# Kernel optimization log

Hardware: AMD Instinct MI355X
Metric: run time of the kernel (lower is better)

Reference implementation:

```python
import jax, jax.numpy as jnp
import numpy as np

DT = 0.1  # fixed RK4 step size from the constructor

def setup_inputs() -> dict:
    key = jax.random.key(0)
    k1, k2, k3 = jax.random.split(key, 3)
    B, U, H = 65536, 128, 512
    x0 = jax.random.normal(k1, (B, U), dtype=jnp.float32)
    # small init so 20 unrolled RK4 steps stay numerically tame
    W1 = jax.random.normal(k2, (U, H), dtype=jnp.float32) * (0.5 / np.sqrt(U))
    b1 = jnp.zeros((H,), dtype=jnp.float32)
    W2 = jax.random.normal(k3, (H, U), dtype=jnp.float32) * (0.5 / np.sqrt(H))
    b2 = jnp.zeros((U,), dtype=jnp.float32)
    return {"x0": x0, "W1": W1, "b1": b1, "W2": W2, "b2": b2}

def _mlp(x, W1, b1, W2, b2):
    # vector field: Dense(512, relu) -> Dense(128); time-independent
    return jnp.maximum(x @ W1 + b1, 0.0) @ W2 + b2

def _rk4_integrate(x, n_steps, W1, b1, W2, b2):
    def step(x, _):
        k1 = _mlp(x, W1, b1, W2, b2)
        k2 = _mlp(x + 0.5 * DT * k1, W1, b1, W2, b2)
        k3 = _mlp(x + 0.5 * DT * k2, W1, b1, W2, b2)
        k4 = _mlp(x + DT * k3, W1, b1, W2, b2)
        return x + (DT / 6.0) * (k1 + 2.0 * k2 + 2.0 * k3 + k4), None
    x, _ = jax.lax.scan(step, x, None, length=n_steps)
    return x

def reference(x0, W1, b1, W2, b2):
    # phase 1: integrate t in [0, t1/2 = 1.0] -> 10 RK4 steps at dt=0.1
    x = _rk4_integrate(x0, 10, W1, b1, W2, b2)
    # phase 2: n=5 macro-steps of length (1.0 - 0.0)/5 = 0.2 -> 2 RK4 steps each
    def macro(x, _):
        x = _rk4_integrate(x, 2, W1, b1, W2, b2)
        return x, None
    x, _ = jax.lax.scan(macro, x, None, length=5)
    return x
```

## Files before the change

### kernel.cpp

```cpp
#include <hip/hip_runtime.h>
#include <stdint.h>


typedef _Float16 half8 __attribute__((ext_vector_type(8)));
typedef float f32x4 __attribute__((ext_vector_type(4)));
typedef __attribute__((address_space(3))) char lchar;
typedef __attribute__((address_space(1))) char gchar;

#define XSTR 136
#define HSTR 40

static __device__ __forceinline__ void gload_lds16(const void* g, void* l) {
  __builtin_amdgcn_global_load_lds((const gchar*)g, (lchar*)l, 16, 0, 0);
}

static __device__ __forceinline__ unsigned short f2h(float x) {
  union { _Float16 h; unsigned short u; } cv;
  cv.h = (_Float16)x;
  return cv.u;
}
static __device__ __forceinline__ float h2f(unsigned short u) {
  union { unsigned short u; _Float16 h; } cv;
  cv.u = u;
  return (float)cv.h;
}
static __device__ __forceinline__ uint64_t pack4(float a, float b, float c, float d) {
  union { _Float16 h[4]; uint64_t q; } cv;
  cv.h[0] = (_Float16)a; cv.h[1] = (_Float16)b;
  cv.h[2] = (_Float16)c; cv.h[3] = (_Float16)d;
  return cv.q;
}

__global__ void pack_w(const float* __restrict__ W1, const float* __restrict__ W2,
                       unsigned short* __restrict__ wp) {
  int id = blockIdx.x * 256 + threadIdx.x;
  int lane = id & 63, fid = (id >> 6) & 255;
  int g = lane >> 4, lm = lane & 15;
  int c = fid >> 4, f = fid & 15;
  if (f < 8) {
    int T = f >> 2, ks = f & 3;
    int hid = c * 32 + T * 16 + lm;
#pragma unroll
    for (int j = 0; j < 8; ++j) {
      int kin = ks * 32 + g * 8 + j;
      wp[fid * 512 + lane * 8 + j] = f2h(W1[kin * 512 + hid]);
    }
  } else {
    int O = f - 8;
    int of = O * 16 + lm;
#pragma unroll
    for (int j = 0; j < 8; ++j) {
      int kh = c * 32 + g * 8 + j;
      wp[fid * 512 + lane * 8 + j] = f2h(W2[kh * 128 + of]);
    }
  }
}

__global__ __launch_bounds__(512, 2) void node_rk4(
    const float* __restrict__ x0, const float* __restrict__ b1,
    const float* __restrict__ b2, const unsigned short* __restrict__ wp,
    float* __restrict__ out) {
  __shared__ char Wbuf[4][16384];
  __shared__ __align__(16) unsigned short xs[8][32][XSTR];
  __shared__ __align__(16) unsigned short hst[8][32][HSTR];
  __shared__ float b1s[512];
  __shared__ float b2s[128];

  const int tid = threadIdx.x;
  const int w = tid >> 6, lane = tid & 63;
  const int g = lane >> 4, lm = lane & 15;

  b1s[tid] = b1[tid];
  if (tid < 128) b2s[tid] = b2[tid];

  const int rbase = blockIdx.x * 256 + w * 32;
  f32x4 xa[2][8];
  ushort4 xbh[2][8];
#pragma unroll
  for (int nt = 0; nt < 2; ++nt)
#pragma unroll
    for (int O = 0; O < 8; ++O) {
      f32x4 v = *(const f32x4*)&x0[(rbase + nt * 16 + lm) * 128 + O * 16 + 4 * g];
      xa[nt][O] = v;
      uint64_t q = pack4(v[0], v[1], v[2], v[3]);
      ushort4 hq;
      *(uint64_t*)&hq = q;
      xbh[nt][O] = hq;
      *(uint64_t*)&xs[w][nt * 16 + lm][O * 16 + 4 * g] = q;
    }

#pragma unroll
  for (int pc = 0; pc < 2; ++pc) {
    const char* src = (const char*)wp + pc * 16384;
#pragma unroll
    for (int q = 0; q < 2; ++q) {
      int seg = w * 2 + q;
      gload_lds16(src + seg * 1024 + lane * 16, Wbuf[pc] + seg * 1024);
    }
  }
  asm volatile("s_waitcnt vmcnt(2) lgkmcnt(0)" ::: "memory");
  __builtin_amdgcn_s_barrier();

#pragma unroll 1
  for (int it = 0; it < 80; ++it) {
    const int s = it & 3;
    const float wgt = (s == 0 || s == 3) ? (0.1f / 6.0f) : (0.1f / 3.0f);
    const float alph = (s < 2) ? 0.05f : 0.1f;

    half8 X1[2][4];
#pragma unroll
    for (int nt = 0; nt < 2; ++nt)
#pragma unroll
      for (int ks = 0; ks < 4; ++ks)
        X1[nt][ks] = *(const half8*)&xs[w][nt * 16 + lm][ks * 32 + g * 8];

    f32x4 yacc[2][8];
#pragma unroll
    for (int nt = 0; nt < 2; ++nt)
#pragma unroll
      for (int O = 0; O < 8; ++O) yacc[nt][O] = f32x4{0.f, 0.f, 0.f, 0.f};

#pragma unroll
    for (int c = 0; c < 16; ++c) {
      half8 Hp0, Hp1;
      if (c > 0) {
        Hp0 = *(const half8*)&hst[w][lm][g * 8];
        Hp1 = *(const half8*)&hst[w][16 + lm][g * 8];
      }

      {
        const int cn = (c + 2) & 15;
        char* buf = Wbuf[(c + 2) & 3];
        const char* src = (const char*)wp + cn * 16384;
#pragma unroll
        for (int q = 0; q < 2; ++q) {
          int seg = w * 2 + q;
          gload_lds16(src + seg * 1024 + lane * 16, buf + seg * 1024);
        }
      }

      __builtin_amdgcn_s_setprio(1);
      if (c > 0) {
        const char* Wp = Wbuf[(c + 3) & 3];
#pragma unroll
        for (int O = 0; O < 8; ++O) {
          half8 wa = *(const half8*)(Wp + 8192 + O * 1024 + lane * 16);
          yacc[0][O] = __builtin_amdgcn_mfma_f32_16x16x32_f16(wa, Hp0, yacc[0][O], 0, 0, 0);
          yacc[1][O] = __builtin_amdgcn_mfma_f32_16x16x32_f16(wa, Hp1, yacc[1][O], 0, 0, 0);
        }
      }

      const char* Wb = Wbuf[c & 3];
#pragma unroll
      for (int T = 0; T < 2; ++T) {
        f32x4 h0 = {0.f, 0.f, 0.f, 0.f}, h1 = {0.f, 0.f, 0.f, 0.f};
#pragma unroll
        for (int ks = 0; ks < 4; ++ks) {
          half8 wa = *(const half8*)(Wb + (T * 4 + ks) * 1024 + lane * 16);
          h0 = __builtin_amdgcn_mfma_f32_16x16x32_f16(wa, X1[0][ks], h0, 0, 0, 0);
          h1 = __builtin_amdgcn_mfma_f32_16x16x32_f16(wa, X1[1][ks], h1, 0, 0, 0);
        }
        __builtin_amdgcn_s_setprio(0);
        f32x4 bb = *(const f32x4*)&b1s[c * 32 + T * 16 + 4 * g];
        uint64_t p0 = pack4(fmaxf(h0[0] + bb[0], 0.f), fmaxf(h0[1] + bb[1], 0.f),
                            fmaxf(h0[2] + bb[2], 0.f), fmaxf(h0[3] + bb[3], 0.f));
        uint64_t p1 = pack4(fmaxf(h1[0] + bb[0], 0.f), fmaxf(h1[1] + bb[1], 0.f),
                            fmaxf(h1[2] + bb[2], 0.f), fmaxf(h1[3] + bb[3], 0.f));
        *(uint64_t*)&hst[w][lm][T * 16 + 4 * g] = p0;
        *(uint64_t*)&hst[w][16 + lm][T * 16 + 4 * g] = p1;
        __builtin_amdgcn_s_setprio(1);
      }
      __builtin_amdgcn_s_setprio(0);

      asm volatile("s_waitcnt vmcnt(2)" ::: "memory");
      __builtin_amdgcn_s_barrier();
    }

    {
      half8 Hl0 = *(const half8*)&hst[w][lm][g * 8];
      half8 Hl1 = *(const half8*)&hst[w][16 + lm][g * 8];
      const char* Wp = Wbuf[3];
#pragma unroll
      for (int O = 0; O < 8; ++O) {
        half8 wa = *(const half8*)(Wp + 8192 + O * 1024 + lane * 16);
        yacc[0][O] = __builtin_amdgcn_mfma_f32_16x16x32_f16(wa, Hl0, yacc[0][O], 0, 0, 0);
        yacc[1][O] = __builtin_amdgcn_mfma_f32_16x16x32_f16(wa, Hl1, yacc[1][O], 0, 0, 0);
      }
    }

#pragma unroll
    for (int nt = 0; nt < 2; ++nt)
#pragma unroll
      for (int O = 0; O < 8; ++O) {
        f32x4 bb2 = *(const f32x4*)&b2s[O * 16 + 4 * g];
        f32x4 k = yacc[nt][O];
#pragma unroll
        for (int j = 0; j < 4; ++j) k[j] += bb2[j];
        xa[nt][O] += wgt * k;
        uint64_t q;
        if (s == 3) {
          f32x4 v = xa[nt][O];
          q = pack4(v[0], v[1], v[2], v[3]);
          ushort4 hq;
          *(uint64_t*)&hq = q;
          xbh[nt][O] = hq;
        } else {
          ushort4 xq = xbh[nt][O];
          q = pack4(h2f(xq.x) + alph * k[0], h2f(xq.y) + alph * k[1],
                    h2f(xq.z) + alph * k[2], h2f(xq.w) + alph * k[3]);
        }
        *(uint64_t*)&xs[w][nt * 16 + lm][O * 16 + 4 * g] = q;
      }
  }

#pragma unroll
  for (int nt = 0; nt < 2; ++nt)
#pragma unroll
    for (int O = 0; O < 8; ++O)
      *(f32x4*)&out[(rbase + nt * 16 + lm) * 128 + O * 16 + 4 * g] = xa[nt][O];
}

extern "C" void kernel_launch(void* const* d_in, const int* in_sizes, int n_in,
                              void* d_out, int out_size, void* d_ws, size_t ws_size,
                              hipStream_t stream) {
  const float* x0 = (const float*)d_in[0];
  const float* W1 = (const float*)d_in[1];
  const float* b1 = (const float*)d_in[2];
  const float* W2 = (const float*)d_in[3];
  const float* b2 = (const float*)d_in[4];
  float* out = (float*)d_out;

  unsigned short* wp = (unsigned short*)d_ws;

  pack_w<<<64, 256, 0, stream>>>(W1, W2, wp);
  node_rk4<<<256, 512, 0, stream>>>(x0, b1, b2, wp, out);
}
```

Before: 1.930 ms.

## Switch MFMA tiles from 16x16x32 to 32x32x16 with repacked weight layout

Replaces the 16x16x32 f16 MFMA tiling with 32x32x16 MFMAs for both MLP layers. The weight packing, the accumulator layout, the x and hidden LDS indexing, and the output mapping are all rewritten to match the 32-row fragment layout. Larger MFMA tiles halve the instruction count and cut LDS operand traffic per FLOP. In exchange, each wave needs more accumulator registers and the epilogue layout changes.

```diff
diff --git a/kernel.cpp b/kernel.cpp
--- a/kernel.cpp
+++ b/kernel.cpp
@@ -4,6 +4,7 @@
 
 typedef _Float16 half8 __attribute__((ext_vector_type(8)));
 typedef float f32x4 __attribute__((ext_vector_type(4)));
+typedef float f32x16 __attribute__((ext_vector_type(16)));
 typedef __attribute__((address_space(3))) char lchar;
 typedef __attribute__((address_space(1))) char gchar;
 
@@ -35,22 +36,21 @@
                        unsigned short* __restrict__ wp) {
   int id = blockIdx.x * 256 + threadIdx.x;
   int lane = id & 63, fid = (id >> 6) & 255;
-  int g = lane >> 4, lm = lane & 15;
+  int n32 = lane & 31, hi = lane >> 5;
   int c = fid >> 4, f = fid & 15;
   if (f < 8) {
-    int T = f >> 2, ks = f & 3;
-    int hid = c * 32 + T * 16 + lm;
+    int hid = c * 32 + n32;
 #pragma unroll
     for (int j = 0; j < 8; ++j) {
-      int kin = ks * 32 + g * 8 + j;
+      int kin = f * 16 + hi * 8 + j;
       wp[fid * 512 + lane * 8 + j] = f2h(W1[kin * 512 + hid]);
     }
   } else {
-    int O = f - 8;
-    int of = O * 16 + lm;
+    int u = f - 8, O = u >> 1, kf = u & 1;
+    int of = O * 32 + n32;
 #pragma unroll
     for (int j = 0; j < 8; ++j) {
-      int kh = c * 32 + g * 8 + j;
+      int kh = c * 32 + kf * 16 + hi * 8 + j;
       wp[fid * 512 + lane * 8 + j] = f2h(W2[kh * 128 + of]);
     }
   }
@@ -68,25 +68,25 @@
 
   const int tid = threadIdx.x;
   const int w = tid >> 6, lane = tid & 63;
-  const int g = lane >> 4, lm = lane & 15;
+  const int n32 = lane & 31, hi = lane >> 5;
 
   b1s[tid] = b1[tid];
   if (tid < 128) b2s[tid] = b2[tid];
 
   const int rbase = blockIdx.x * 256 + w * 32;
-  f32x4 xa[2][8];
-  ushort4 xbh[2][8];
-#pragma unroll
-  for (int nt = 0; nt < 2; ++nt)
-#pragma unroll
-    for (int O = 0; O < 8; ++O) {
-      f32x4 v = *(const f32x4*)&x0[(rbase + nt * 16 + lm) * 128 + O * 16 + 4 * g];
-      xa[nt][O] = v;
-      uint64_t q = pack4(v[0], v[1], v[2], v[3]);
+  f32x4 xa[4][4];
+  ushort4 xbh[4][4];
+#pragma unroll
+  for (int O = 0; O < 4; ++O)
+#pragma unroll
+    for (int q = 0; q < 4; ++q) {
+      f32x4 v = *(const f32x4*)&x0[(rbase + n32) * 128 + O * 32 + 8 * q + 4 * hi];
+      xa[O][q] = v;
+      uint64_t qq = pack4(v[0], v[1], v[2], v[3]);
       ushort4 hq;
-      *(uint64_t*)&hq = q;
-      xbh[nt][O] = hq;
-      *(uint64_t*)&xs[w][nt * 16 + lm][O * 16 + 4 * g] = q;
+      *(uint64_t*)&hq = qq;
+      xbh[O][q] = hq;
+      *(uint64_t*)&xs[w][n32][O * 32 + 8 * q + 4 * hi] = qq;
     }
 
 #pragma unroll
@@ -107,25 +107,23 @@
     const float wgt = (s == 0 || s == 3) ? (0.1f / 6.0f) : (0.1f / 3.0f);
     const float alph = (s < 2) ? 0.05f : 0.1f;
 
-    half8 X1[2][4];
-#pragma unroll
-    for (int nt = 0; nt < 2; ++nt)
-#pragma unroll
-      for (int ks = 0; ks < 4; ++ks)
-        X1[nt][ks] = *(const half8*)&xs[w][nt * 16 + lm][ks * 32 + g * 8];
-
-    f32x4 yacc[2][8];
-#pragma unroll
-    for (int nt = 0; nt < 2; ++nt)
-#pragma unroll
-      for (int O = 0; O < 8; ++O) yacc[nt][O] = f32x4{0.f, 0.f, 0.f, 0.f};
+    half8 X1[8];
+#pragma unroll
+    for (int ks = 0; ks < 8; ++ks)
+      X1[ks] = *(const half8*)&xs[w][n32][ks * 16 + hi * 8];
+
+    f32x16 yacc[4];
+#pragma unroll
+    for (int O = 0; O < 4; ++O)
+#pragma unroll
+      for (int e = 0; e < 16; ++e) yacc[O][e] = 0.f;
 
 #pragma unroll
     for (int c = 0; c < 16; ++c) {
       half8 Hp0, Hp1;
       if (c > 0) {
-        Hp0 = *(const half8*)&hst[w][lm][g * 8];
-        Hp1 = *(const half8*)&hst[w][16 + lm][g * 8];
+        Hp0 = *(const half8*)&hst[w][n32][hi * 8];
+        Hp1 = *(const half8*)&hst[w][n32][16 + hi * 8];
       }
 
       {
@@ -143,81 +141,82 @@
       if (c > 0) {
         const char* Wp = Wbuf[(c + 3) & 3];
 #pragma unroll
-        for (int O = 0; O < 8; ++O) {
-          half8 wa = *(const half8*)(Wp + 8192 + O * 1024 + lane * 16);
-          yacc[0][O] = __builtin_amdgcn_mfma_f32_16x16x32_f16(wa, Hp0, yacc[0][O], 0, 0, 0);
-          yacc[1][O] = __builtin_amdgcn_mfma_f32_16x16x32_f16(wa, Hp1, yacc[1][O], 0, 0, 0);
+        for (int O = 0; O < 4; ++O) {
+          half8 wa0 = *(const half8*)(Wp + 8192 + (O * 2 + 0) * 1024 + lane * 16);
+          half8 wa1 = *(const half8*)(Wp + 8192 + (O * 2 + 1) * 1024 + lane * 16);
+          yacc[O] = __builtin_amdgcn_mfma_f32_32x32x16_f16(wa0, Hp0, yacc[O], 0, 0, 0);
+          yacc[O] = __builtin_amdgcn_mfma_f32_32x32x16_f16(wa1, Hp1, yacc[O], 0, 0, 0);
         }
       }
 
       const char* Wb = Wbuf[c & 3];
-#pragma unroll
-      for (int T = 0; T < 2; ++T) {
-        f32x4 h0 = {0.f, 0.f, 0.f, 0.f}, h1 = {0.f, 0.f, 0.f, 0.f};
-#pragma unroll
-        for (int ks = 0; ks < 4; ++ks) {
-          half8 wa = *(const half8*)(Wb + (T * 4 + ks) * 1024 + lane * 16);
-          h0 = __builtin_amdgcn_mfma_f32_16x16x32_f16(wa, X1[0][ks], h0, 0, 0, 0);
-          h1 = __builtin_amdgcn_mfma_f32_16x16x32_f16(wa, X1[1][ks], h1, 0, 0, 0);
-        }
-        __builtin_amdgcn_s_setprio(0);
-        f32x4 bb = *(const f32x4*)&b1s[c * 32 + T * 16 + 4 * g];
-        uint64_t p0 = pack4(fmaxf(h0[0] + bb[0], 0.f), fmaxf(h0[1] + bb[1], 0.f),
-                            fmaxf(h0[2] + bb[2], 0.f), fmaxf(h0[3] + bb[3], 0.f));
-        uint64_t p1 = pack4(fmaxf(h1[0] + bb[0], 0.f), fmaxf(h1[1] + bb[1], 0.f),
-                            fmaxf(h1[2] + bb[2], 0.f), fmaxf(h1[3] + bb[3], 0.f));
-        *(uint64_t*)&hst[w][lm][T * 16 + 4 * g] = p0;
-        *(uint64_t*)&hst[w][16 + lm][T * 16 + 4 * g] = p1;
-        __builtin_amdgcn_s_setprio(1);
+      f32x16 hacc;
+#pragma unroll
+      for (int e = 0; e < 16; ++e) hacc[e] = 0.f;
+#pragma unroll
+      for (int ks = 0; ks < 8; ++ks) {
+        half8 wa = *(const half8*)(Wb + ks * 1024 + lane * 16);
+        hacc = __builtin_amdgcn_mfma_f32_32x32x16_f16(wa, X1[ks], hacc, 0, 0, 0);
       }
       __builtin_amdgcn_s_setprio(0);
+
+#pragma unroll
+      for (int q = 0; q < 4; ++q) {
+        f32x4 bb = *(const f32x4*)&b1s[c * 32 + 8 * q + 4 * hi];
+        uint64_t p = pack4(fmaxf(hacc[4 * q + 0] + bb[0], 0.f),
+                           fmaxf(hacc[4 * q + 1] + bb[1], 0.f),
+                           fmaxf(hacc[4 * q + 2] + bb[2], 0.f),
+                           fmaxf(hacc[4 * q + 3] + bb[3], 0.f));
+        *(uint64_t*)&hst[w][n32][8 * q + 4 * hi] = p;
+      }
 
       asm volatile("s_waitcnt vmcnt(2)" ::: "memory");
       __builtin_amdgcn_s_barrier();
     }
 
     {
-      half8 Hl0 = *(const half8*)&hst[w][lm][g * 8];
-      half8 Hl1 = *(const half8*)&hst[w][16 + lm][g * 8];
+      half8 Hl0 = *(const half8*)&hst[w][n32][hi * 8];
+      half8 Hl1 = *(const half8*)&hst[w][n32][16 + hi * 8];
       const char* Wp = Wbuf[3];
 #pragma unroll
-      for (int O = 0; O < 8; ++O) {
-        half8 wa = *(const half8*)(Wp + 8192 + O * 1024 + lane * 16);
-        yacc[0][O] = __builtin_amdgcn_mfma_f32_16x16x32_f16(wa, Hl0, yacc[0][O], 0, 0, 0);
-        yacc[1][O] = __builtin_amdgcn_mfma_f32_16x16x32_f16(wa, Hl1, yacc[1][O], 0, 0, 0);
-      }
-    }
-
-#pragma unroll
-    for (int nt = 0; nt < 2; ++nt)
-#pragma unroll
-      for (int O = 0; O < 8; ++O) {
-        f32x4 bb2 = *(const f32x4*)&b2s[O * 16 + 4 * g];
-        f32x4 k = yacc[nt][O];
-#pragma unroll
-        for (int j = 0; j < 4; ++j) k[j] += bb2[j];
-        xa[nt][O] += wgt * k;
-        uint64_t q;
+      for (int O = 0; O < 4; ++O) {
+        half8 wa0 = *(const half8*)(Wp + 8192 + (O * 2 + 0) * 1024 + lane * 16);
+        half8 wa1 = *(const half8*)(Wp + 8192 + (O * 2 + 1) * 1024 + lane * 16);
+        yacc[O] = __builtin_amdgcn_mfma_f32_32x32x16_f16(wa0, Hl0, yacc[O], 0, 0, 0);
+        yacc[O] = __builtin_amdgcn_mfma_f32_32x32x16_f16(wa1, Hl1, yacc[O], 0, 0, 0);
+      }
+    }
+
+#pragma unroll
+    for (int O = 0; O < 4; ++O)
+#pragma unroll
+      for (int q = 0; q < 4; ++q) {
+        f32x4 bb2 = *(const f32x4*)&b2s[O * 32 + 8 * q + 4 * hi];
+        f32x4 k;
+#pragma unroll
+        for (int j = 0; j < 4; ++j) k[j] = yacc[O][4 * q + j] + bb2[j];
+        xa[O][q] += wgt * k;
+        uint64_t qq;
         if (s == 3) {
-          f32x4 v = xa[nt][O];
-          q = pack4(v[0], v[1], v[2], v[3]);
+          f32x4 v = xa[O][q];
+          qq = pack4(v[0], v[1], v[2], v[3]);
           ushort4 hq;
-          *(uint64_t*)&hq = q;
-          xbh[nt][O] = hq;
+          *(uint64_t*)&hq = qq;
+          xbh[O][q] = hq;
         } else {
-          ushort4 xq = xbh[nt][O];
-          q = pack4(h2f(xq.x) + alph * k[0], h2f(xq.y) + alph * k[1],
-                    h2f(xq.z) + alph * k[2], h2f(xq.w) + alph * k[3]);
+          ushort4 xq = xbh[O][q];
+          qq = pack4(h2f(xq.x) + alph * k[0], h2f(xq.y) + alph * k[1],
+                     h2f(xq.z) + alph * k[2], h2f(xq.w) + alph * k[3]);
         }
-        *(uint64_t*)&xs[w][nt * 16 + lm][O * 16 + 4 * g] = q;
+        *(uint64_t*)&xs[w][n32][O * 32 + 8 * q + 4 * hi] = qq;
       }
   }
 
 #pragma unroll
-  for (int nt = 0; nt < 2; ++nt)
-#pragma unroll
-    for (int O = 0; O < 8; ++O)
-      *(f32x4*)&out[(rbase + nt * 16 + lm) * 128 + O * 16 + 4 * g] = xa[nt][O];
+  for (int O = 0; O < 4; ++O)
+#pragma unroll
+    for (int q = 0; q < 4; ++q)
+      *(f32x4*)&out[(rbase + n32) * 128 + O * 32 + 8 * q + 4 * hi] = xa[O][q];
 }
 
 extern "C" void kernel_launch(void* const* d_in, const int* in_sizes, int n_in,
```

Result: slower. 2.156 ms (+11.7%).

## Give each wave 64 rows with 4 waves per block and swizzle LDS tiles

Applied to the files above, without the earlier changes.

Blocks shrink from 8 waves to 4, and each wave now processes 64 batch rows instead of 32, so every weight fragment read from LDS feeds four MFMAs instead of two. The LDS tiles for x and h drop their padded strides in favor of an XOR swizzle to avoid bank conflicts, and the s_setprio hints are removed. The cost is much higher register pressure from the larger accumulator, x and hidden arrays. Fewer waves are also available to hide the per-chunk barrier and global-to-LDS weight loads, and register spills are possible.

```diff
diff --git a/kernel.cpp b/kernel.cpp
--- a/kernel.cpp
+++ b/kernel.cpp
@@ -6,9 +6,6 @@
 typedef float f32x4 __attribute__((ext_vector_type(4)));
 typedef __attribute__((address_space(3))) char lchar;
 typedef __attribute__((address_space(1))) char gchar;
-
-#define XSTR 136
-#define HSTR 40
 
 static __device__ __forceinline__ void gload_lds16(const void* g, void* l) {
   __builtin_amdgcn_global_load_lds((const gchar*)g, (lchar*)l, 16, 0, 0);
@@ -29,6 +26,13 @@
   cv.h[0] = (_Float16)a; cv.h[1] = (_Float16)b;
   cv.h[2] = (_Float16)c; cv.h[3] = (_Float16)d;
   return cv.q;
+}
+
+static __device__ __forceinline__ int xs_off(int r, int feat) {
+  return (r * 272 + feat * 2) ^ ((r & 8) << 1);
+}
+static __device__ __forceinline__ int hs_off(int r, int hid) {
+  return (r * 80 + hid * 2) ^ ((r & 8) << 1);
 }
 
 __global__ void pack_w(const float* __restrict__ W1, const float* __restrict__ W2,
@@ -56,28 +60,31 @@
   }
 }
 
-__global__ __launch_bounds__(512, 2) void node_rk4(
+__global__ __launch_bounds__(256, 1) void node_rk4(
     const float* __restrict__ x0, const float* __restrict__ b1,
     const float* __restrict__ b2, const unsigned short* __restrict__ wp,
     float* __restrict__ out) {
   __shared__ char Wbuf[4][16384];
-  __shared__ __align__(16) unsigned short xs[8][32][XSTR];
-  __shared__ __align__(16) unsigned short hst[8][32][HSTR];
+  __shared__ __align__(16) char xsm[4][64 * 272];
+  __shared__ __align__(16) char hsm[4][64 * 80];
   __shared__ float b1s[512];
   __shared__ float b2s[128];
 
   const int tid = threadIdx.x;
   const int w = tid >> 6, lane = tid & 63;
   const int g = lane >> 4, lm = lane & 15;
+  char* xsw = xsm[w];
+  char* hsw = hsm[w];
 
   b1s[tid] = b1[tid];
+  b1s[tid + 256] = b1[tid + 256];
   if (tid < 128) b2s[tid] = b2[tid];
 
-  const int rbase = blockIdx.x * 256 + w * 32;
-  f32x4 xa[2][8];
-  ushort4 xbh[2][8];
-#pragma unroll
-  for (int nt = 0; nt < 2; ++nt)
+  const int rbase = blockIdx.x * 256 + w * 64;
+  f32x4 xa[4][8];
+  ushort4 xbh[4][8];
+#pragma unroll
+  for (int nt = 0; nt < 4; ++nt)
 #pragma unroll
     for (int O = 0; O < 8; ++O) {
       f32x4 v = *(const f32x4*)&x0[(rbase + nt * 16 + lm) * 128 + O * 16 + 4 * g];
@@ -86,19 +93,20 @@
       ushort4 hq;
       *(uint64_t*)&hq = q;
       xbh[nt][O] = hq;
-      *(uint64_t*)&xs[w][nt * 16 + lm][O * 16 + 4 * g] = q;
+      int r = nt * 16 + lm;
+      *(uint64_t*)(xsw + xs_off(r, O * 16 + 4 * g)) = q;
     }
 
 #pragma unroll
   for (int pc = 0; pc < 2; ++pc) {
     const char* src = (const char*)wp + pc * 16384;
 #pragma unroll
-    for (int q = 0; q < 2; ++q) {
-      int seg = w * 2 + q;
+    for (int q = 0; q < 4; ++q) {
+      int seg = w * 4 + q;
       gload_lds16(src + seg * 1024 + lane * 16, Wbuf[pc] + seg * 1024);
     }
   }
-  asm volatile("s_waitcnt vmcnt(2) lgkmcnt(0)" ::: "memory");
+  asm volatile("s_waitcnt vmcnt(4) lgkmcnt(0)" ::: "memory");
   __builtin_amdgcn_s_barrier();
 
 #pragma unroll 1
@@ -107,25 +115,27 @@
     const float wgt = (s == 0 || s == 3) ? (0.1f / 6.0f) : (0.1f / 3.0f);
     const float alph = (s < 2) ? 0.05f : 0.1f;
 
-    half8 X1[2][4];
-#pragma unroll
-    for (int nt = 0; nt < 2; ++nt)
+    half8 X1[4][4];
+#pragma unroll
+    for (int nt = 0; nt < 4; ++nt)
 #pragma unroll
       for (int ks = 0; ks < 4; ++ks)
-        X1[nt][ks] = *(const half8*)&xs[w][nt * 16 + lm][ks * 32 + g * 8];
-
-    f32x4 yacc[2][8];
-#pragma unroll
-    for (int nt = 0; nt < 2; ++nt)
+        X1[nt][ks] =
+            *(const half8*)(xsw + xs_off(nt * 16 + lm, ks * 32 + g * 8));
+
+    f32x4 yacc[4][8];
+#pragma unroll
+    for (int nt = 0; nt < 4; ++nt)
 #pragma unroll
       for (int O = 0; O < 8; ++O) yacc[nt][O] = f32x4{0.f, 0.f, 0.f, 0.f};
 
 #pragma unroll
     for (int c = 0; c < 16; ++c) {
-      half8 Hp0, Hp1;
+      half8 Hp[4];
       if (c > 0) {
-        Hp0 = *(const half8*)&hst[w][lm][g * 8];
-        Hp1 = *(const half8*)&hst[w][16 + lm][g * 8];
+#pragma unroll
+        for (int nt = 0; nt < 4; ++nt)
+          Hp[nt] = *(const half8*)(hsw + hs_off(nt * 16 + lm, g * 8));
       }
 
       {
@@ -133,63 +143,68 @@
         char* buf = Wbuf[(c + 2) & 3];
         const char* src = (const char*)wp + cn * 16384;
 #pragma unroll
-        for (int q = 0; q < 2; ++q) {
-          int seg = w * 2 + q;
+        for (int q = 0; q < 4; ++q) {
+          int seg = w * 4 + q;
           gload_lds16(src + seg * 1024 + lane * 16, buf + seg * 1024);
         }
       }
 
-      __builtin_amdgcn_s_setprio(1);
       if (c > 0) {
         const char* Wp = Wbuf[(c + 3) & 3];
 #pragma unroll
         for (int O = 0; O < 8; ++O) {
           half8 wa = *(const half8*)(Wp + 8192 + O * 1024 + lane * 16);
-          yacc[0][O] = __builtin_amdgcn_mfma_f32_16x16x32_f16(wa, Hp0, yacc[0][O], 0, 0, 0);
-          yacc[1][O] = __builtin_amdgcn_mfma_f32_16x16x32_f16(wa, Hp1, yacc[1][O], 0, 0, 0);
+#pragma unroll
+          for (int nt = 0; nt < 4; ++nt)
+            yacc[nt][O] =
+                __builtin_amdgcn_mfma_f32_16x16x32_f16(wa, Hp[nt], yacc[nt][O], 0, 0, 0);
         }
       }
 
       const char* Wb = Wbuf[c & 3];
 #pragma unroll
       for (int T = 0; T < 2; ++T) {
-        f32x4 h0 = {0.f, 0.f, 0.f, 0.f}, h1 = {0.f, 0.f, 0.f, 0.f};
+        f32x4 hc[4];
+#pragma unroll
+        for (int nt = 0; nt < 4; ++nt) hc[nt] = f32x4{0.f, 0.f, 0.f, 0.f};
 #pragma unroll
         for (int ks = 0; ks < 4; ++ks) {
           half8 wa = *(const half8*)(Wb + (T * 4 + ks) * 1024 + lane * 16);
-          h0 = __builtin_amdgcn_mfma_f32_16x16x32_f16(wa, X1[0][ks], h0, 0, 0, 0);
-          h1 = __builtin_amdgcn_mfma_f32_16x16x32_f16(wa, X1[1][ks], h1, 0, 0, 0);
-        }
-        __builtin_amdgcn_s_setprio(0);
+#pragma unroll
+          for (int nt = 0; nt < 4; ++nt)
+            hc[nt] = __builtin_amdgcn_mfma_f32_16x16x32_f16(wa, X1[nt][ks], hc[nt], 0, 0, 0);
+        }
         f32x4 bb = *(const f32x4*)&b1s[c * 32 + T * 16 + 4 * g];
-        uint64_t p0 = pack4(fmaxf(h0[0] + bb[0], 0.f), fmaxf(h0[1] + bb[1], 0.f),
-                            fmaxf(h0[2] + bb[2], 0.f), fmaxf(h0[3] + bb[3], 0.f));
-        uint64_t p1 = pack4(fmaxf(h1[0] + bb[0], 0.f), fmaxf(h1[1] + bb[1], 0.f),
-                            fmaxf(h1[2] + bb[2], 0.f), fmaxf(h1[3] + bb[3], 0.f));
-        *(uint64_t*)&hst[w][lm][T * 16 + 4 * g] = p0;
-        *(uint64_t*)&hst[w][16 + lm][T * 16 + 4 * g] = p1;
-        __builtin_amdgcn_s_setprio(1);
-      }
-      __builtin_amdgcn_s_setprio(0);
-
-      asm volatile("s_waitcnt vmcnt(2)" ::: "memory");
+#pragma unroll
+        for (int nt = 0; nt < 4; ++nt) {
+          uint64_t p = pack4(fmaxf(hc[nt][0] + bb[0], 0.f), fmaxf(hc[nt][1] + bb[1], 0.f),
+                             fmaxf(hc[nt][2] + bb[2], 0.f), fmaxf(hc[nt][3] + bb[3], 0.f));
+          *(uint64_t*)(hsw + hs_off(nt * 16 + lm, T * 16 + 4 * g)) = p;
+        }
+      }
+
+      asm volatile("s_waitcnt vmcnt(4)" ::: "memory");
       __builtin_amdgcn_s_barrier();
     }
 
     {
-      half8 Hl0 = *(const half8*)&hst[w][lm][g * 8];
-      half8 Hl1 = *(const half8*)&hst[w][16 + lm][g * 8];
+      half8 Hl[4];
+#pragma unroll
+      for (int nt = 0; nt < 4; ++nt)
+        Hl[nt] = *(const half8*)(hsw + hs_off(nt * 16 + lm, g * 8));
       const char* Wp = Wbuf[3];
 #pragma unroll
       for (int O = 0; O < 8; ++O) {
         half8 wa = *(const half8*)(Wp + 8192 + O * 1024 + lane * 16);
-        yacc[0][O] = __builtin_amdgcn_mfma_f32_16x16x32_f16(wa, Hl0, yacc[0][O], 0, 0, 0);
-        yacc[1][O] = __builtin_amdgcn_mfma_f32_16x16x32_f16(wa, Hl1, yacc[1][O], 0, 0, 0);
-      }
-    }
-
-#pragma unroll
-    for (int nt = 0; nt < 2; ++nt)
+#pragma unroll
+        for (int nt = 0; nt < 4; ++nt)
+          yacc[nt][O] =
+              __builtin_amdgcn_mfma_f32_16x16x32_f16(wa, Hl[nt], yacc[nt][O], 0, 0, 0);
+      }
+    }
+
+#pragma unroll
+    for (int nt = 0; nt < 4; ++nt)
 #pragma unroll
       for (int O = 0; O < 8; ++O) {
         f32x4 bb2 = *(const f32x4*)&b2s[O * 16 + 4 * g];
@@ -209,12 +224,12 @@
           q = pack4(h2f(xq.x) + alph * k[0], h2f(xq.y) + alph * k[1],
                     h2f(xq.z) + alph * k[2], h2f(xq.w) + alph * k[3]);
         }
-        *(uint64_t*)&xs[w][nt * 16 + lm][O * 16 + 4 * g] = q;
+        *(uint64_t*)(xsw + xs_off(nt * 16 + lm, O * 16 + 4 * g)) = q;
       }
   }
 
 #pragma unroll
-  for (int nt = 0; nt < 2; ++nt)
+  for (int nt = 0; nt < 4; ++nt)
 #pragma unroll
     for (int O = 0; O < 8; ++O)
       *(f32x4*)&out[(rbase + nt * 16 + lm) * 128 + O * 16 + 4 * g] = xa[nt][O];
@@ -233,5 +248,5 @@
   unsigned short* wp = (unsigned short*)d_ws;
 
   pack_w<<<64, 256, 0, stream>>>(W1, W2, wp);
-  node_rk4<<<256, 512, 0, stream>>>(x0, b1, b2, wp, out);
-}
+  node_rk4<<<256, 256, 0, stream>>>(x0, b1, b2, wp, out);
+}
```

After: 4.411 ms. +128.6%, slower.

## Keep hidden activations in registers by swapping MFMA operand roles for layer two

Applied to the files above, without the earlier changes.

The second-layer MFMA now takes the packed ReLU hidden tile straight from registers as the A operand, with W2 as the B operand. W2 is repacked with a permuted k-index so the accumulator layout of layer one lines up with the operand layout of layer two. This removes the hst shared-memory round trip (store, then reload) for every hidden chunk. In exchange the output accumulators become transposed, so the x state is written to LDS as scalar 2-byte stores spread across rows, and global loads and stores become strided scalar accesses instead of 16-byte vectors.

```diff
diff --git a/kernel.cpp b/kernel.cpp
--- a/kernel.cpp
+++ b/kernel.cpp
@@ -8,7 +8,6 @@
 typedef __attribute__((address_space(1))) char gchar;
 
 #define XSTR 136
-#define HSTR 40
 
 static __device__ __forceinline__ void gload_lds16(const void* g, void* l) {
   __builtin_amdgcn_global_load_lds((const gchar*)g, (lchar*)l, 16, 0, 0);
@@ -50,8 +49,8 @@
     int of = O * 16 + lm;
 #pragma unroll
     for (int j = 0; j < 8; ++j) {
-      int kh = c * 32 + g * 8 + j;
-      wp[fid * 512 + lane * 8 + j] = f2h(W2[kh * 128 + of]);
+      int khl = (j < 4) ? (4 * g + j) : (16 + 4 * g + (j - 4));
+      wp[fid * 512 + lane * 8 + j] = f2h(W2[(c * 32 + khl) * 128 + of]);
     }
   }
 }
@@ -62,7 +61,6 @@
     float* __restrict__ out) {
   __shared__ char Wbuf[4][16384];
   __shared__ __align__(16) unsigned short xs[8][32][XSTR];
-  __shared__ __align__(16) unsigned short hst[8][32][HSTR];
   __shared__ float b1s[512];
   __shared__ float b2s[128];
 
@@ -77,16 +75,19 @@
   f32x4 xa[2][8];
   ushort4 xbh[2][8];
 #pragma unroll
-  for (int nt = 0; nt < 2; ++nt)
+  for (int mt = 0; mt < 2; ++mt)
 #pragma unroll
     for (int O = 0; O < 8; ++O) {
-      f32x4 v = *(const f32x4*)&x0[(rbase + nt * 16 + lm) * 128 + O * 16 + 4 * g];
-      xa[nt][O] = v;
-      uint64_t q = pack4(v[0], v[1], v[2], v[3]);
+      f32x4 v;
+#pragma unroll
+      for (int j = 0; j < 4; ++j)
+        v[j] = x0[(rbase + mt * 16 + 4 * g + j) * 128 + O * 16 + lm];
+      xa[mt][O] = v;
       ushort4 hq;
-      *(uint64_t*)&hq = q;
-      xbh[nt][O] = hq;
-      *(uint64_t*)&xs[w][nt * 16 + lm][O * 16 + 4 * g] = q;
+      hq.x = f2h(v[0]); hq.y = f2h(v[1]); hq.z = f2h(v[2]); hq.w = f2h(v[3]);
+      xbh[mt][O] = hq;
+      unsigned short* xr = &xs[w][mt * 16 + 4 * g][O * 16 + lm];
+      xr[0] = hq.x; xr[XSTR] = hq.y; xr[2 * XSTR] = hq.z; xr[3 * XSTR] = hq.w;
     }
 
 #pragma unroll
@@ -116,18 +117,14 @@
 
     f32x4 yacc[2][8];
 #pragma unroll
-    for (int nt = 0; nt < 2; ++nt)
-#pragma unroll
-      for (int O = 0; O < 8; ++O) yacc[nt][O] = f32x4{0.f, 0.f, 0.f, 0.f};
+    for (int mt = 0; mt < 2; ++mt)
+#pragma unroll
+      for (int O = 0; O < 8; ++O) yacc[mt][O] = f32x4{0.f, 0.f, 0.f, 0.f};
+
+    half8 hpk[2][2];
 
 #pragma unroll
     for (int c = 0; c < 16; ++c) {
-      half8 Hp0, Hp1;
-      if (c > 0) {
-        Hp0 = *(const half8*)&hst[w][lm][g * 8];
-        Hp1 = *(const half8*)&hst[w][16 + lm][g * 8];
-      }
-
       {
         const int cn = (c + 2) & 15;
         char* buf = Wbuf[(c + 2) & 3];
@@ -144,80 +141,97 @@
         const char* Wp = Wbuf[(c + 3) & 3];
 #pragma unroll
         for (int O = 0; O < 8; ++O) {
-          half8 wa = *(const half8*)(Wp + 8192 + O * 1024 + lane * 16);
-          yacc[0][O] = __builtin_amdgcn_mfma_f32_16x16x32_f16(wa, Hp0, yacc[0][O], 0, 0, 0);
-          yacc[1][O] = __builtin_amdgcn_mfma_f32_16x16x32_f16(wa, Hp1, yacc[1][O], 0, 0, 0);
+          half8 w2f = *(const half8*)(Wp + 8192 + O * 1024 + lane * 16);
+          yacc[0][O] = __builtin_amdgcn_mfma_f32_16x16x32_f16(hpk[(c - 1) & 1][0], w2f,
+                                                              yacc[0][O], 0, 0, 0);
+          yacc[1][O] = __builtin_amdgcn_mfma_f32_16x16x32_f16(hpk[(c - 1) & 1][1], w2f,
+                                                              yacc[1][O], 0, 0, 0);
         }
       }
 
       const char* Wb = Wbuf[c & 3];
-#pragma unroll
-      for (int T = 0; T < 2; ++T) {
-        f32x4 h0 = {0.f, 0.f, 0.f, 0.f}, h1 = {0.f, 0.f, 0.f, 0.f};
+      f32x4 hacc[2][2];
+#pragma unroll
+      for (int T = 0; T < 2; ++T)
+#pragma unroll
+        for (int nt = 0; nt < 2; ++nt) hacc[T][nt] = f32x4{0.f, 0.f, 0.f, 0.f};
+#pragma unroll
+      for (int T = 0; T < 2; ++T)
 #pragma unroll
         for (int ks = 0; ks < 4; ++ks) {
           half8 wa = *(const half8*)(Wb + (T * 4 + ks) * 1024 + lane * 16);
-          h0 = __builtin_amdgcn_mfma_f32_16x16x32_f16(wa, X1[0][ks], h0, 0, 0, 0);
-          h1 = __builtin_amdgcn_mfma_f32_16x16x32_f16(wa, X1[1][ks], h1, 0, 0, 0);
-        }
-        __builtin_amdgcn_s_setprio(0);
-        f32x4 bb = *(const f32x4*)&b1s[c * 32 + T * 16 + 4 * g];
-        uint64_t p0 = pack4(fmaxf(h0[0] + bb[0], 0.f), fmaxf(h0[1] + bb[1], 0.f),
-                            fmaxf(h0[2] + bb[2], 0.f), fmaxf(h0[3] + bb[3], 0.f));
-        uint64_t p1 = pack4(fmaxf(h1[0] + bb[0], 0.f), fmaxf(h1[1] + bb[1], 0.f),
-                            fmaxf(h1[2] + bb[2], 0.f), fmaxf(h1[3] + bb[3], 0.f));
-        *(uint64_t*)&hst[w][lm][T * 16 + 4 * g] = p0;
-        *(uint64_t*)&hst[w][16 + lm][T * 16 + 4 * g] = p1;
-        __builtin_amdgcn_s_setprio(1);
-      }
+          hacc[T][0] =
+              __builtin_amdgcn_mfma_f32_16x16x32_f16(wa, X1[0][ks], hacc[T][0], 0, 0, 0);
+          hacc[T][1] =
+              __builtin_amdgcn_mfma_f32_16x16x32_f16(wa, X1[1][ks], hacc[T][1], 0, 0, 0);
+        }
       __builtin_amdgcn_s_setprio(0);
+
+      f32x4 bb0 = *(const f32x4*)&b1s[c * 32 + 4 * g];
+      f32x4 bb1 = *(const f32x4*)&b1s[c * 32 + 16 + 4 * g];
+#pragma unroll
+      for (int nt = 0; nt < 2; ++nt) {
+        union { uint64_t q[2]; half8 h; } u;
+        u.q[0] = pack4(fmaxf(hacc[0][nt][0] + bb0[0], 0.f),
+                       fmaxf(hacc[0][nt][1] + bb0[1], 0.f),
+                       fmaxf(hacc[0][nt][2] + bb0[2], 0.f),
+                       fmaxf(hacc[0][nt][3] + bb0[3], 0.f));
+        u.q[1] = pack4(fmaxf(hacc[1][nt][0] + bb1[0], 0.f),
+                       fmaxf(hacc[1][nt][1] + bb1[1], 0.f),
+                       fmaxf(hacc[1][nt][2] + bb1[2], 0.f),
+                       fmaxf(hacc[1][nt][3] + bb1[3], 0.f));
+        hpk[c & 1][nt] = u.h;
+      }
 
       asm volatile("s_waitcnt vmcnt(2)" ::: "memory");
       __builtin_amdgcn_s_barrier();
     }
 
     {
-      half8 Hl0 = *(const half8*)&hst[w][lm][g * 8];
-      half8 Hl1 = *(const half8*)&hst[w][16 + lm][g * 8];
       const char* Wp = Wbuf[3];
 #pragma unroll
       for (int O = 0; O < 8; ++O) {
-        half8 wa = *(const half8*)(Wp + 8192 + O * 1024 + lane * 16);
-        yacc[0][O] = __builtin_amdgcn_mfma_f32_16x16x32_f16(wa, Hl0, yacc[0][O], 0, 0, 0);
-        yacc[1][O] = __builtin_amdgcn_mfma_f32_16x16x32_f16(wa, Hl1, yacc[1][O], 0, 0, 0);
-      }
-    }
-
-#pragma unroll
-    for (int nt = 0; nt < 2; ++nt)
+        half8 w2f = *(const half8*)(Wp + 8192 + O * 1024 + lane * 16);
+        yacc[0][O] =
+            __builtin_amdgcn_mfma_f32_16x16x32_f16(hpk[1][0], w2f, yacc[0][O], 0, 0, 0);
+        yacc[1][O] =
+            __builtin_amdgcn_mfma_f32_16x16x32_f16(hpk[1][1], w2f, yacc[1][O], 0, 0, 0);
+      }
+    }
+
+#pragma unroll
+    for (int mt = 0; mt < 2; ++mt)
 #pragma unroll
       for (int O = 0; O < 8; ++O) {
-        f32x4 bb2 = *(const f32x4*)&b2s[O * 16 + 4 * g];
-        f32x4 k = yacc[nt][O];
-#pragma unroll
-        for (int j = 0; j < 4; ++j) k[j] += bb2[j];
-        xa[nt][O] += wgt * k;
-        uint64_t q;
+        float bb2 = b2s[O * 16 + lm];
+        f32x4 k = yacc[mt][O];
+#pragma unroll
+        for (int j = 0; j < 4; ++j) k[j] += bb2;
+        xa[mt][O] += wgt * k;
+        ushort4 hq;
         if (s == 3) {
-          f32x4 v = xa[nt][O];
-          q = pack4(v[0], v[1], v[2], v[3]);
-          ushort4 hq;
-          *(uint64_t*)&hq = q;
-          xbh[nt][O] = hq;
+          f32x4 v = xa[mt][O];
+          hq.x = f2h(v[0]); hq.y = f2h(v[1]); hq.z = f2h(v[2]); hq.w = f2h(v[3]);
+          xbh[mt][O] = hq;
         } else {
-          ushort4 xq = xbh[nt][O];
-          q = pack4(h2f(xq.x) + alph * k[0], h2f(xq.y) + alph * k[1],
-                    h2f(xq.z) + alph * k[2], h2f(xq.w) + alph * k[3]);
-        }
-        *(uint64_t*)&xs[w][nt * 16 + lm][O * 16 + 4 * g] = q;
+          ushort4 xq = xbh[mt][O];
+          hq.x = f2h(h2f(xq.x) + alph * k[0]);
+          hq.y = f2h(h2f(xq.y) + alph * k[1]);
+          hq.z = f2h(h2f(xq.z) + alph * k[2]);
+          hq.w = f2h(h2f(xq.w) + alph * k[3]);
+        }
+        unsigned short* xr = &xs[w][mt * 16 + 4 * g][O * 16 + lm];
+        xr[0] = hq.x; xr[XSTR] = hq.y; xr[2 * XSTR] = hq.z; xr[3 * XSTR] = hq.w;
       }
   }
 
 #pragma unroll
-  for (int nt = 0; nt < 2; ++nt)
+  for (int mt = 0; mt < 2; ++mt)
 #pragma unroll
     for (int O = 0; O < 8; ++O)
-      *(f32x4*)&out[(rbase + nt * 16 + lm) * 128 + O * 16 + 4 * g] = xa[nt][O];
+#pragma unroll
+      for (int j = 0; j < 4; ++j)
+        out[(rbase + mt * 16 + 4 * g + j) * 128 + O * 16 + lm] = xa[mt][O][j];
 }
 
 extern "C" void kernel_launch(void* const* d_in, const int* in_sizes, int n_in,
```

After: 2.159 ms. 1.12x slower.
